# Kernel optimization log

Hardware: AMD Instinct MI355X
Metric: run time of the kernel (lower is better)

The kernel has to match this reference:

```python
import jax, jax.numpy as jnp
import numpy as np

T, B, IN, H = 512, 64, 1024, 1024


def setup_inputs() -> dict:
    key = jax.random.key(0)
    kx, kwx, kwh, kb = jax.random.split(key, 4)
    x = jax.random.normal(kx, (T, B, IN), dtype=jnp.float32)
    # xavier_normal for 2D params: std = sqrt(2/(fan_in+fan_out))
    Wxh = jax.random.normal(kwx, (H, IN), dtype=jnp.float32) * np.sqrt(2.0 / (H + IN))
    Whh = jax.random.normal(kwh, (H, H), dtype=jnp.float32) * np.sqrt(2.0 / (H + H))
    bh = jax.random.normal(kb, (H,), dtype=jnp.float32)
    return {"x": x, "Wxh": Wxh, "Whh": Whh, "bh": bh}


def reference(x, Wxh, Whh, bh):
    # Precompute input projection for all timesteps in one batched GEMM.
    xproj = jnp.einsum('tbi,hi->tbh', x, Wxh) + bh  # [T, B, H]
    WhhT = Whh.T
    h0 = jnp.zeros((x.shape[1], Whh.shape[0]), dtype=x.dtype)

    def step(h, xp_t):
        h_new = jnp.tanh(xp_t + h @ WhhT)
        return h_new, h_new

    h_last, out = jax.lax.scan(step, h0, xproj)
    return out, h_last
```

## Files before the change

### kernel.cpp

```cpp
#include <hip/hip_runtime.h>


typedef _Float16 f16;
typedef _Float16 f16x8 __attribute__((ext_vector_type(8)));
typedef float f32x4 __attribute__((ext_vector_type(4)));
typedef unsigned int u32;
typedef unsigned long long u64;

#define T_STEPS 512
#define NB 64
#define NH 1024
#define ROWP 1040

__device__ __forceinline__ f16x8 cvt8(const float4 a, const float4 b) {
    f16x8 v;
    v[0] = (f16)a.x; v[1] = (f16)a.y; v[2] = (f16)a.z; v[3] = (f16)a.w;
    v[4] = (f16)b.x; v[5] = (f16)b.y; v[6] = (f16)b.z; v[7] = (f16)b.w;
    return v;
}

__device__ __forceinline__ float fast_tanh(float x) {
    float e = __expf(2.0f * x);
    return 1.0f - 2.0f / (e + 1.0f);
}

extern "C" __global__ void __launch_bounds__(256, 1)
rnn_persist(const float* __restrict__ x, const float* __restrict__ Wxh,
            const float* __restrict__ Whh, const float* __restrict__ bh,
            float* __restrict__ out, float* __restrict__ hglob,
            u32* __restrict__ flags)
{
    __shared__ __align__(16) f16 xlds[2][4 * ROWP];
    __shared__ __align__(16) f16 hlds[4 * ROWP];

    const int tid  = threadIdx.x;
    const int lane = tid & 63;
    const int wv   = tid >> 6;
    const int g    = (lane >> 4) & 3;
    const int l15  = lane & 15;

    const int bidx    = blockIdx.x;
    const int cluster = ((bidx & 7) << 1) | ((bidx >> 3) & 1);
    const int member  = bidx >> 4;
    const int bbase   = cluster * 4;
    const int n       = member * 64 + wv * 16 + l15;

    f16x8 bx[32], bw[32];
#pragma unroll
    for (int kt = 0; kt < 32; ++kt) {
        const float* px = Wxh + (size_t)n * NH + kt * 32 + g * 8;
        const float* pw = Whh + (size_t)n * NH + kt * 32 + g * 8;
        float4 a0 = ((const float4*)px)[0], a1 = ((const float4*)px)[1];
        float4 c0 = ((const float4*)pw)[0], c1 = ((const float4*)pw)[1];
        bx[kt] = cvt8(a0, a1);
        bw[kt] = cvt8(c0, c1);
    }
    const float bias = bh[n];

    const int sb = wv;
    const float* xsrc0 = x + (size_t)(bbase + sb) * NH + lane * 16;
    f16* xd0  = &xlds[0][sb * ROWP + lane * 16];
    f16* xd1  = &xlds[1][sb * ROWP + lane * 16];
    f16* hdst = &hlds[sb * ROWP + lane * 16];

    const f16* xa0 = &xlds[0][(l15 & 3) * ROWP + g * 8];
    const f16* xa1 = &xlds[1][(l15 & 3) * ROWP + g * 8];
    const f16* ha  = &hlds[(l15 & 3) * ROWP + g * 8];

    float4 xr0, xr1, xr2, xr3;
    u64 hv[8];
    const u64* hb = (const u64*)hglob;
    u32* hgu = (u32*)hglob;

    f32x4 acc[8];
    float hvv[4];

    auto load_x = [&](int t) {
        const float4* p = (const float4*)(xsrc0 + (size_t)t * (NB * NH));
        xr0 = p[0]; xr1 = p[1]; xr2 = p[2]; xr3 = p[3];
    };
    auto write_x = [&](int par) {
        f16* d = par ? xd1 : xd0;
        *(f16x8*)d       = cvt8(xr0, xr1);
        *(f16x8*)(d + 8) = cvt8(xr2, xr3);
    };
    auto stage_h_load = [&](int par) {
        const u64* s = hb + ((size_t)(par * NB + bbase + sb)) * (NH / 2) + (size_t)lane * 8;
#pragma unroll
        for (int i = 0; i < 8; ++i)
            hv[i] = __hip_atomic_load(s + i, __ATOMIC_RELAXED, __HIP_MEMORY_SCOPE_AGENT);
    };
    auto stage_h_write = [&]() {
        f16x8 lo, hi;
#pragma unroll
        for (int i = 0; i < 4; ++i) {
            float2 p0 = __builtin_bit_cast(float2, hv[i]);
            float2 p1 = __builtin_bit_cast(float2, hv[4 + i]);
            lo[2 * i] = (f16)p0.x; lo[2 * i + 1] = (f16)p0.y;
            hi[2 * i] = (f16)p1.x; hi[2 * i + 1] = (f16)p1.y;
        }
        *(f16x8*)hdst       = lo;
        *(f16x8*)(hdst + 8) = hi;
    };
    auto zero_acc = [&]() {
#pragma unroll
        for (int i = 0; i < 8; ++i) acc[i] = f32x4{0.f, 0.f, 0.f, 0.f};
    };
    auto mfma_x = [&](const f16* xa) {
#pragma unroll
        for (int kt = 0; kt < 32; ++kt)
            acc[kt & 7] = __builtin_amdgcn_mfma_f32_16x16x32_f16(
                *(const f16x8*)(xa + kt * 32), bx[kt], acc[kt & 7], 0, 0, 0);
    };
    auto mfma_h = [&]() {
#pragma unroll
        for (int kt = 0; kt < 32; ++kt)
            acc[(kt + 4) & 7] = __builtin_amdgcn_mfma_f32_16x16x32_f16(
                *(const f16x8*)(ha + kt * 32), bw[kt], acc[(kt + 4) & 7], 0, 0, 0);
    };
    auto compute_h = [&](int t) {
        f32x4 s = ((acc[0] + acc[1]) + (acc[2] + acc[3])) +
                  ((acc[4] + acc[5]) + (acc[6] + acc[7]));
        if (lane < 16) {
            const int par = (t + 1) & 1;
#pragma unroll
            for (int r = 0; r < 4; ++r) {
                hvv[r] = fast_tanh(s[r] + bias);
                const size_t idx = ((size_t)par * NB + bbase + r) * NH + n;
                __hip_atomic_store(hgu + idx, __builtin_bit_cast(u32, hvv[r]),
                                   __ATOMIC_RELAXED, __HIP_MEMORY_SCOPE_AGENT);
            }
        }
    };
    auto out_stores = [&](int t) {
        if (lane < 16) {
#pragma unroll
            for (int r = 0; r < 4; ++r) {
                const int b = bbase + r;
                __builtin_nontemporal_store(hvv[r], out + ((size_t)t * NB + b) * NH + n);
                if (t == T_STEPS - 1)
                    __builtin_nontemporal_store(
                        hvv[r], out + (size_t)T_STEPS * NB * NH + (size_t)b * NH + n);
            }
        }
    };
    u32* flagp = flags + cluster * 256 + member * 16;
    const u32* fpoll = flags + cluster * 256 + l15 * 16;
    auto poll = [&](u32 target) {
        int guard = 1 << 16;
        for (;;) {
            u32 v = __hip_atomic_load(fpoll, __ATOMIC_RELAXED, __HIP_MEMORY_SCOPE_AGENT);
            if (__all((int)(v >= target))) break;
            if (--guard == 0) break;
            __builtin_amdgcn_s_sleep(1);
        }
        asm volatile("" ::: "memory");
    };

    load_x(0); write_x(0);
    load_x(1);
    __syncthreads();
    zero_acc();
    mfma_x(xa0);
    compute_h(0);
    asm volatile("s_waitcnt vmcnt(0)" ::: "memory");
    write_x(1);
    __syncthreads();
    if (tid == 0)
        __hip_atomic_store(flagp, 1u, __ATOMIC_RELAXED, __HIP_MEMORY_SCOPE_AGENT);
    out_stores(0);
    poll(1);

    for (int t = 1; t < T_STEPS; ++t) {
        const int par = t & 1;
        stage_h_load(par);
        zero_acc();
        mfma_x(par ? xa1 : xa0);
        stage_h_write();
        if (t < T_STEPS - 1) load_x(t + 1);
        __syncthreads();
        mfma_h();
        compute_h(t);
        asm volatile("s_waitcnt vmcnt(0)" ::: "memory");
        if (t < T_STEPS - 1) write_x((t + 1) & 1);
        __syncthreads();
        if (t < T_STEPS - 1) {
            if (tid == 0)
                __hip_atomic_store(flagp, (u32)(t + 1), __ATOMIC_RELAXED,
                                   __HIP_MEMORY_SCOPE_AGENT);
            out_stores(t);
            poll((u32)(t + 1));
        } else {
            out_stores(t);
        }
    }
}

extern "C" void kernel_launch(void* const* d_in, const int* in_sizes, int n_in,
                              void* d_out, int out_size, void* d_ws, size_t ws_size,
                              hipStream_t stream) {
    const float* x   = (const float*)d_in[0];
    const float* Wxh = (const float*)d_in[1];
    const float* Whh = (const float*)d_in[2];
    const float* bh  = (const float*)d_in[3];
    float* out       = (float*)d_out;
    float* hglob     = (float*)d_ws;
    u32* flags       = (u32*)((char*)d_ws + 524288);
    hipMemsetAsync(flags, 0, 16 * 16 * 64, stream);
    rnn_persist<<<dim3(256), dim3(256), 0, stream>>>(x, Wxh, Whh, bh, out, hglob, flags);
}
```

Before: 2.324 ms.

## Replace flag-based step sync with step-tagged f16 hidden-state words

Each hidden value is now published to global memory as one 32-bit word: the f16 value in the low half and the timestep tag in the high half. Consumers spin on the data words themselves until every tag matches, which removes the separate flag store, the flag poll and the extra load round trip, along with the flag memset. The step loop is also reordered so the next step's input-projection MFMAs and a deeper x prefetch run before the hidden-state poll, overlapping them with the cross-block wait. In exchange it relies on stale tags in the uninitialized workspace never matching the expected step, and it spins without sleeping, which adds memory traffic while polling.

```diff
diff --git a/kernel.cpp b/kernel.cpp
--- a/kernel.cpp
+++ b/kernel.cpp
@@ -5,7 +5,7 @@
 typedef _Float16 f16x8 __attribute__((ext_vector_type(8)));
 typedef float f32x4 __attribute__((ext_vector_type(4)));
 typedef unsigned int u32;
-typedef unsigned long long u64;
+typedef unsigned short u16;
 
 #define T_STEPS 512
 #define NB 64
@@ -24,11 +24,14 @@
     return 1.0f - 2.0f / (e + 1.0f);
 }
 
+__device__ __forceinline__ void lds_barrier() {
+    asm volatile("s_waitcnt lgkmcnt(0)\ns_barrier" ::: "memory");
+}
+
 extern "C" __global__ void __launch_bounds__(256, 1)
 rnn_persist(const float* __restrict__ x, const float* __restrict__ Wxh,
             const float* __restrict__ Whh, const float* __restrict__ bh,
-            float* __restrict__ out, float* __restrict__ hglob,
-            u32* __restrict__ flags)
+            float* __restrict__ out, u32* __restrict__ hglob)
 {
     __shared__ __align__(16) f16 xlds[2][4 * ROWP];
     __shared__ __align__(16) f16 hlds[4 * ROWP];
@@ -68,10 +71,7 @@
     const f16* ha  = &hlds[(l15 & 3) * ROWP + g * 8];
 
     float4 xr0, xr1, xr2, xr3;
-    u64 hv[8];
-    const u64* hb = (const u64*)hglob;
-    u32* hgu = (u32*)hglob;
-
+    u32 w[16];
     f32x4 acc[8];
     float hvv[4];
 
@@ -83,24 +83,6 @@
         f16* d = par ? xd1 : xd0;
         *(f16x8*)d       = cvt8(xr0, xr1);
         *(f16x8*)(d + 8) = cvt8(xr2, xr3);
-    };
-    auto stage_h_load = [&](int par) {
-        const u64* s = hb + ((size_t)(par * NB + bbase + sb)) * (NH / 2) + (size_t)lane * 8;
-#pragma unroll
-        for (int i = 0; i < 8; ++i)
-            hv[i] = __hip_atomic_load(s + i, __ATOMIC_RELAXED, __HIP_MEMORY_SCOPE_AGENT);
-    };
-    auto stage_h_write = [&]() {
-        f16x8 lo, hi;
-#pragma unroll
-        for (int i = 0; i < 4; ++i) {
-            float2 p0 = __builtin_bit_cast(float2, hv[i]);
-            float2 p1 = __builtin_bit_cast(float2, hv[4 + i]);
-            lo[2 * i] = (f16)p0.x; lo[2 * i + 1] = (f16)p0.y;
-            hi[2 * i] = (f16)p1.x; hi[2 * i + 1] = (f16)p1.y;
-        }
-        *(f16x8*)hdst       = lo;
-        *(f16x8*)(hdst + 8) = hi;
     };
     auto zero_acc = [&]() {
 #pragma unroll
@@ -118,6 +100,30 @@
             acc[(kt + 4) & 7] = __builtin_amdgcn_mfma_f32_16x16x32_f16(
                 *(const f16x8*)(ha + kt * 32), bw[kt], acc[(kt + 4) & 7], 0, 0, 0);
     };
+    auto poll_h = [&](int t) {
+        const u32* s = hglob + ((size_t)((t & 1) * NB + bbase + sb)) * NH + lane * 16;
+        int guard = 1 << 16;
+        for (;;) {
+            bool ok = true;
+#pragma unroll
+            for (int i = 0; i < 16; ++i) {
+                w[i] = __hip_atomic_load(s + i, __ATOMIC_RELAXED, __HIP_MEMORY_SCOPE_AGENT);
+                ok &= ((w[i] >> 16) == (u32)t);
+            }
+            if (__all(ok)) break;
+            if (--guard == 0) break;
+        }
+    };
+    auto stage_h_write = [&]() {
+        f16x8 lo, hi;
+#pragma unroll
+        for (int i = 0; i < 8; ++i) {
+            lo[i] = __builtin_bit_cast(f16, (u16)(w[i] & 0xffffu));
+            hi[i] = __builtin_bit_cast(f16, (u16)(w[8 + i] & 0xffffu));
+        }
+        *(f16x8*)hdst       = lo;
+        *(f16x8*)(hdst + 8) = hi;
+    };
     auto compute_h = [&](int t) {
         f32x4 s = ((acc[0] + acc[1]) + (acc[2] + acc[3])) +
                   ((acc[4] + acc[5]) + (acc[6] + acc[7]));
@@ -125,10 +131,15 @@
             const int par = (t + 1) & 1;
 #pragma unroll
             for (int r = 0; r < 4; ++r) {
-                hvv[r] = fast_tanh(s[r] + bias);
-                const size_t idx = ((size_t)par * NB + bbase + r) * NH + n;
-                __hip_atomic_store(hgu + idx, __builtin_bit_cast(u32, hvv[r]),
-                                   __ATOMIC_RELAXED, __HIP_MEMORY_SCOPE_AGENT);
+                float hv = fast_tanh(s[r] + bias);
+                hvv[r] = hv;
+                if (t < T_STEPS - 1) {
+                    u32 word = ((u32)(t + 1) << 16) |
+                               (u32)__builtin_bit_cast(u16, (f16)hv);
+                    __hip_atomic_store(
+                        hglob + ((size_t)par * NB + bbase + r) * NH + n, word,
+                        __ATOMIC_RELAXED, __HIP_MEMORY_SCOPE_AGENT);
+                }
             }
         }
     };
@@ -144,54 +155,30 @@
             }
         }
     };
-    u32* flagp = flags + cluster * 256 + member * 16;
-    const u32* fpoll = flags + cluster * 256 + l15 * 16;
-    auto poll = [&](u32 target) {
-        int guard = 1 << 16;
-        for (;;) {
-            u32 v = __hip_atomic_load(fpoll, __ATOMIC_RELAXED, __HIP_MEMORY_SCOPE_AGENT);
-            if (__all((int)(v >= target))) break;
-            if (--guard == 0) break;
-            __builtin_amdgcn_s_sleep(1);
-        }
-        asm volatile("" ::: "memory");
-    };
 
     load_x(0); write_x(0);
     load_x(1);
-    __syncthreads();
+    lds_barrier();
+    write_x(1);
+    load_x(2);
     zero_acc();
     mfma_x(xa0);
-    compute_h(0);
-    asm volatile("s_waitcnt vmcnt(0)" ::: "memory");
-    write_x(1);
-    __syncthreads();
-    if (tid == 0)
-        __hip_atomic_store(flagp, 1u, __ATOMIC_RELAXED, __HIP_MEMORY_SCOPE_AGENT);
-    out_stores(0);
-    poll(1);
 
-    for (int t = 1; t < T_STEPS; ++t) {
-        const int par = t & 1;
-        stage_h_load(par);
-        zero_acc();
-        mfma_x(par ? xa1 : xa0);
-        stage_h_write();
-        if (t < T_STEPS - 1) load_x(t + 1);
-        __syncthreads();
-        mfma_h();
+    for (int t = 0; t < T_STEPS; ++t) {
+        if (t > 0) {
+            poll_h(t);
+            stage_h_write();
+        }
+        lds_barrier();
+        if (t > 0) mfma_h();
         compute_h(t);
-        asm volatile("s_waitcnt vmcnt(0)" ::: "memory");
-        if (t < T_STEPS - 1) write_x((t + 1) & 1);
-        __syncthreads();
+        out_stores(t);
         if (t < T_STEPS - 1) {
-            if (tid == 0)
-                __hip_atomic_store(flagp, (u32)(t + 1), __ATOMIC_RELAXED,
-                                   __HIP_MEMORY_SCOPE_AGENT);
-            out_stores(t);
-            poll((u32)(t + 1));
-        } else {
-            out_stores(t);
+            zero_acc();
+            mfma_x(((t + 1) & 1) ? xa1 : xa0);
+            if (t <= T_STEPS - 3) write_x(t & 1);
+            if (t <= T_STEPS - 4) load_x(t + 3);
+            lds_barrier();
         }
     }
 }
@@ -204,8 +191,6 @@
     const float* Whh = (const float*)d_in[2];
     const float* bh  = (const float*)d_in[3];
     float* out       = (float*)d_out;
-    float* hglob     = (float*)d_ws;
-    u32* flags       = (u32*)((char*)d_ws + 524288);
-    hipMemsetAsync(flags, 0, 16 * 16 * 64, stream);
-    rnn_persist<<<dim3(256), dim3(256), 0, stream>>>(x, Wxh, Whh, bh, out, hglob, flags);
+    u32* hglob       = (u32*)d_ws;
+    rnn_persist<<<dim3(256), dim3(256), 0, stream>>>(x, Wxh, Whh, bh, out, hglob);
 }
```

Result: slower. 2.696 ms (+16.0%).
